# Kernel optimization log

Hardware: AMD Instinct MI355X
Metric: run time of the kernel (lower is better)

Reference implementation:

```python
import jax, jax.numpy as jnp
import numpy as np

H = 16
D_MODEL = 1024
D_K = D_MODEL // H
NWORDS = 16384


def setup_inputs() -> dict:
    key0 = jax.random.key(0)
    ks = jax.random.split(key0, 11)
    s = 0.02
    return {
        "query": jax.random.normal(ks[0], (1, D_MODEL), dtype=jnp.float32),
        "key": jax.random.normal(ks[1], (NWORDS, D_MODEL), dtype=jnp.float32),
        "value": jax.random.normal(ks[2], (NWORDS, D_MODEL), dtype=jnp.float32),
        "Wq": jax.random.normal(ks[3], (D_MODEL, D_MODEL), dtype=jnp.float32) * s,
        "bq": jax.random.normal(ks[4], (D_MODEL,), dtype=jnp.float32) * s,
        "Wk": jax.random.normal(ks[5], (D_MODEL, D_MODEL), dtype=jnp.float32) * s,
        "bk": jax.random.normal(ks[6], (D_MODEL,), dtype=jnp.float32) * s,
        "Wv": jax.random.normal(ks[7], (D_MODEL, D_MODEL), dtype=jnp.float32) * s,
        "bv": jax.random.normal(ks[8], (D_MODEL,), dtype=jnp.float32) * s,
        "Wo": jax.random.normal(ks[9], (D_MODEL, D_MODEL), dtype=jnp.float32) * s,
        "bo": jax.random.normal(ks[10], (D_MODEL,), dtype=jnp.float32) * s,
    }


def reference(query, key, value, Wq, bq, Wk, bk, Wv, bv, Wo, bo):
    # torch Linear: y = x @ W.T + b
    q = (query @ Wq.T + bq).reshape(H, D_K)          # [h, d_k]  (single query token)
    k = (key @ Wk.T + bk).reshape(-1, H, D_K)        # [n, h, d_k]
    v = (value @ Wv.T + bv).reshape(-1, H, D_K)      # [n, h, d_k]
    # NOTE: original module applies NO 1/sqrt(d_k) scaling.
    scores = jnp.einsum("hd,nhd->hn", q, k)          # [h, n]
    p_attn = jax.nn.softmax(scores, axis=-1)          # dropout p=0 -> no-op
    x = jnp.einsum("hn,nhd->hd", p_attn, v).reshape(1, H * D_K)  # [1, d_model]
    return x @ Wo.T + bo                              # [1, d_model]
```

## Files before the change

kernel.cpp:

```cpp
#include <hip/hip_runtime.h>

#define DM 1024
#define NW 16384

typedef __attribute__((ext_vector_type(8))) short short8;
typedef __attribute__((ext_vector_type(4))) float f32x4;

#define OFF_AH   1024
#define OFF_AL   9216
#define OFF_D0   17408
#define OFF_S    17424
#define OFF_X    17696
#define OFF_W    18720
#define OFF_PART 36864

__device__ __forceinline__ unsigned short f2bf(float f) {
  unsigned int u = __float_as_uint(f);
  return (unsigned short)((u + 0x7fffu + ((u >> 16) & 1u)) >> 16);
}

__global__ __launch_bounds__(256) void k_rowdot(const float* __restrict__ W,
                                                const float* __restrict__ v,
                                                const float* __restrict__ b,
                                                float* __restrict__ out) {
  const int wave = (blockIdx.x * 256 + threadIdx.x) >> 6;
  const int lane = threadIdx.x & 63;
  const float* row = W + (size_t)wave * DM + 4 * lane;
  float s = 0.f;
#pragma unroll
  for (int j = 0; j < 4; ++j) {
    float4 a = *(const float4*)(row + j * 256);
    float4 x = *(const float4*)(v + j * 256 + 4 * lane);
    s += a.x * x.x + a.y * x.y + a.z * x.z + a.w * x.w;
  }
#pragma unroll
  for (int off = 32; off; off >>= 1) s += __shfl_xor(s, off, 64);
  if (lane == 0) out[wave] = s + b[wave];
}

__global__ __launch_bounds__(256) void k_qck(const float* __restrict__ Wq,
                                             const float* __restrict__ bq,
                                             const float* __restrict__ query,
                                             const float* __restrict__ Wk,
                                             const float* __restrict__ bk,
                                             short* __restrict__ Ah,
                                             short* __restrict__ Al,
                                             float* __restrict__ d0,
                                             float* __restrict__ S,
                                             float* __restrict__ w) {
  const int h = blockIdx.x >> 2;
  const int mc = blockIdx.x & 3;
  const int t = threadIdx.x;
  const int lane = t & 63;
  const int wv = t >> 6;
  __shared__ float qh[64];
  if (blockIdx.x == 0 && t < 16) S[t] = 0.f;
  w[blockIdx.x * 256 + t] = 0.f;
  float4 qv[4];
#pragma unroll
  for (int j = 0; j < 4; ++j) qv[j] = *(const float4*)(query + j * 256 + 4 * lane);
#pragma unroll 1
  for (int ii = 0; ii < 16; ii += 4) {
    float4 a[4][4];
#pragma unroll
    for (int r = 0; r < 4; ++r) {
      const float* rp = Wq + (size_t)(h * 64 + 4 * (ii + r) + wv) * DM + 4 * lane;
#pragma unroll
      for (int j = 0; j < 4; ++j) a[r][j] = *(const float4*)(rp + j * 256);
    }
    float s[4] = {0.f, 0.f, 0.f, 0.f};
#pragma unroll
    for (int r = 0; r < 4; ++r)
#pragma unroll
      for (int j = 0; j < 4; ++j)
        s[r] += a[r][j].x * qv[j].x + a[r][j].y * qv[j].y +
                a[r][j].z * qv[j].z + a[r][j].w * qv[j].w;
#pragma unroll
    for (int off = 32; off; off >>= 1)
#pragma unroll
      for (int r = 0; r < 4; ++r) s[r] += __shfl_xor(s[r], off, 64);
    if (lane == 0)
#pragma unroll
      for (int r = 0; r < 4; ++r)
        qh[4 * (ii + r) + wv] = s[r] + bq[h * 64 + 4 * (ii + r) + wv];
  }
  __syncthreads();
  const int m = mc * 256 + t;
  const float* Wp = Wk + (size_t)(h * 64) * DM + m;
  float s = 0.f;
#pragma unroll 2
  for (int db = 0; db < 8; ++db) {
    float wv8[8];
#pragma unroll
    for (int j = 0; j < 8; ++j) wv8[j] = Wp[(size_t)(db * 8 + j) * DM];
#pragma unroll
    for (int j = 0; j < 8; ++j) s = fmaf(qh[db * 8 + j], wv8[j], s);
  }
  unsigned short hu = f2bf(s);
  float hf = __uint_as_float(((unsigned int)hu) << 16);
  unsigned short lu = f2bf(s - hf);
  const int kb = m >> 5, q = (m >> 3) & 3, j = m & 7;
  const int idx = (kb * 64 + q * 16 + h) * 8 + j;
  Ah[idx] = (short)hu;
  Al[idx] = (short)lu;
  if (mc == 0 && t == 0) {
    float tt = 0.f;
    for (int d = 0; d < 64; ++d) tt += qh[d] * bk[h * 64 + d];
    d0[h] = tt;
  }
}

__global__ __launch_bounds__(256, 1) void k_spv(const float* __restrict__ key,
                                                const float* __restrict__ value,
                                                const short* __restrict__ AhG,
                                                const short* __restrict__ AlG,
                                                const float* __restrict__ d0,
                                                float* __restrict__ part,
                                                float* __restrict__ S) {
  const int nb = blockIdx.x;
  const int t = threadIdx.x;
  const int lane = t & 63;
  const int wv = t >> 6;
  const int nl = wv * 16 + (lane & 15);
  const int n = nb * 64 + nl;
  const int quad = lane >> 4;
  const float* base = key + (size_t)n * DM + quad * 8;
  const short8* A8h = (const short8*)AhG;
  const short8* A8l = (const short8*)AlG;
  __shared__ float el[64 * 16];

  short8 ah[2][4], al[2][4];
  float4 f0[2][4], f1[2][4];
  f32x4 acc0 = {0.f, 0.f, 0.f, 0.f};
  f32x4 acc1 = {0.f, 0.f, 0.f, 0.f};

#define LOADG(buf, g) { \
  _Pragma("unroll") for (int i = 0; i < 4; ++i) { \
    const int kb = (g) * 4 + i; \
    ah[buf][i] = A8h[kb * 64 + lane]; \
    al[buf][i] = A8l[kb * 64 + lane]; \
    f0[buf][i] = *(const float4*)(base + kb * 32); \
    f1[buf][i] = *(const float4*)(base + kb * 32 + 4); \
  } }

#define PROC(buf) { \
  _Pragma("unroll") for (int i = 0; i < 4; ++i) { \
    float ff[8] = {f0[buf][i].x, f0[buf][i].y, f0[buf][i].z, f0[buf][i].w, \
                   f1[buf][i].x, f1[buf][i].y, f1[buf][i].z, f1[buf][i].w}; \
    short8 bh, bl; \
    _Pragma("unroll") for (int j = 0; j < 8; ++j) { \
      unsigned short hu = f2bf(ff[j]); \
      bh[j] = (short)hu; \
      float hf = __uint_as_float(((unsigned int)hu) << 16); \
      bl[j] = (short)f2bf(ff[j] - hf); \
    } \
    if ((i & 1) == 0) { \
      acc0 = __builtin_amdgcn_mfma_f32_16x16x32_bf16(ah[buf][i], bh, acc0, 0, 0, 0); \
      acc0 = __builtin_amdgcn_mfma_f32_16x16x32_bf16(ah[buf][i], bl, acc0, 0, 0, 0); \
      acc0 = __builtin_amdgcn_mfma_f32_16x16x32_bf16(al[buf][i], bh, acc0, 0, 0, 0); \
    } else { \
      acc1 = __builtin_amdgcn_mfma_f32_16x16x32_bf16(ah[buf][i], bh, acc1, 0, 0, 0); \
      acc1 = __builtin_amdgcn_mfma_f32_16x16x32_bf16(ah[buf][i], bl, acc1, 0, 0, 0); \
      acc1 = __builtin_amdgcn_mfma_f32_16x16x32_bf16(al[buf][i], bh, acc1, 0, 0, 0); \
    } \
  } }

  LOADG(0, 0)
  LOADG(1, 1)
  PROC(0) LOADG(0, 2)
  PROC(1) LOADG(1, 3)
  PROC(0) LOADG(0, 4)
  PROC(1) LOADG(1, 5)
  PROC(0) LOADG(0, 6)
  PROC(1) LOADG(1, 7)
  PROC(0)
  PROC(1)
#undef LOADG
#undef PROC

  {
    const float4 dv = *(const float4*)(d0 + quad * 4);
    float ex0 = __expf(acc0[0] + acc1[0] + dv.x);
    float ex1 = __expf(acc0[1] + acc1[1] + dv.y);
    float ex2 = __expf(acc0[2] + acc1[2] + dv.z);
    float ex3 = __expf(acc0[3] + acc1[3] + dv.w);
    *(float4*)&el[nl * 16 + quad * 4] = make_float4(ex0, ex1, ex2, ex3);
  }
  __syncthreads();

  float4 acc[16];
#pragma unroll
  for (int h = 0; h < 16; ++h) acc[h] = make_float4(0.f, 0.f, 0.f, 0.f);
  const float* vp = value + (size_t)(nb * 64) * DM + 4 * t;
#pragma unroll 1
  for (int rb = 0; rb < 8; ++rb) {
    float4 v[8];
#pragma unroll
    for (int i = 0; i < 8; ++i) v[i] = *(const float4*)(vp + (size_t)(rb * 8 + i) * DM);
#pragma unroll
    for (int i = 0; i < 8; ++i) {
      const float4* er4 = (const float4*)&el[(rb * 8 + i) * 16];
      float4 e0 = er4[0], e1 = er4[1], e2 = er4[2], e3 = er4[3];
      float4 vv = v[i];
#define FMA4H(H, P) { acc[H].x = fmaf(P, vv.x, acc[H].x); acc[H].y = fmaf(P, vv.y, acc[H].y); \
                      acc[H].z = fmaf(P, vv.z, acc[H].z); acc[H].w = fmaf(P, vv.w, acc[H].w); }
      FMA4H(0,  e0.x) FMA4H(1,  e0.y) FMA4H(2,  e0.z) FMA4H(3,  e0.w)
      FMA4H(4,  e1.x) FMA4H(5,  e1.y) FMA4H(6,  e1.z) FMA4H(7,  e1.w)
      FMA4H(8,  e2.x) FMA4H(9,  e2.y) FMA4H(10, e2.z) FMA4H(11, e2.w)
      FMA4H(12, e3.x) FMA4H(13, e3.y) FMA4H(14, e3.z) FMA4H(15, e3.w)
#undef FMA4H
    }
  }
  float* pp = part + (size_t)nb * (16 * DM) + 4 * t;
#pragma unroll
  for (int h = 0; h < 16; ++h) *(float4*)(pp + (size_t)h * DM) = acc[h];

  if (t < 16) {
    float s = 0.f;
#pragma unroll
    for (int r = 0; r < 64; ++r) s += el[r * 16 + t];
    atomicAdd(S + t, s);
  }
}

__global__ __launch_bounds__(256) void k_wred(const float* __restrict__ part,
                                              float* __restrict__ w) {
  const int g = blockIdx.x * 256 + threadIdx.x;
  const int o = g & 16383;
  const int q = g >> 14;
  float s = 0.f;
#pragma unroll 1
  for (int ib = 0; ib < 8; ++ib) {
    float x[8];
#pragma unroll
    for (int j = 0; j < 8; ++j)
      x[j] = part[(size_t)(q * 64 + ib * 8 + j) * 16384 + o];
#pragma unroll
    for (int j = 0; j < 8; ++j) s += x[j];
  }
  atomicAdd(w + o, s);
}

__global__ __launch_bounds__(256) void k_xproj(const float* __restrict__ Wv,
                                               const float* __restrict__ w,
                                               const float* __restrict__ bv,
                                               const float* __restrict__ S,
                                               float* __restrict__ x) {
  const int wave = (blockIdx.x * 256 + threadIdx.x) >> 6;
  const int lane = threadIdx.x & 63;
  const int h = wave >> 6;
  const float* vec = w + (size_t)h * DM;
  const float* row = Wv + (size_t)wave * DM + 4 * lane;
  float s = 0.f;
#pragma unroll
  for (int j = 0; j < 4; ++j) {
    float4 a = *(const float4*)(row + j * 256);
    float4 x4 = *(const float4*)(vec + j * 256 + 4 * lane);
    s += a.x * x4.x + a.y * x4.y + a.z * x4.z + a.w * x4.w;
  }
#pragma unroll
  for (int off = 32; off; off >>= 1) s += __shfl_xor(s, off, 64);
  if (lane == 0) x[wave] = s / S[h] + bv[wave];
}

extern "C" void kernel_launch(void* const* d_in, const int* in_sizes, int n_in,
                              void* d_out, int out_size, void* d_ws, size_t ws_size,
                              hipStream_t stream) {
  const float* query = (const float*)d_in[0];
  const float* key   = (const float*)d_in[1];
  const float* value = (const float*)d_in[2];
  const float* Wq    = (const float*)d_in[3];
  const float* bq    = (const float*)d_in[4];
  const float* Wk    = (const float*)d_in[5];
  const float* bk    = (const float*)d_in[6];
  const float* Wv    = (const float*)d_in[7];
  const float* bv    = (const float*)d_in[8];
  const float* Wo    = (const float*)d_in[9];
  const float* bo    = (const float*)d_in[10];
  float* out = (float*)d_out;
  float* ws  = (float*)d_ws;
  short* Ah  = (short*)(ws + OFF_AH);
  short* Al  = (short*)(ws + OFF_AL);

  k_qck    <<<64,  256, 0, stream>>>(Wq, bq, query, Wk, bk, Ah, Al,
                                     ws + OFF_D0, ws + OFF_S, ws + OFF_W);
  k_spv    <<<256, 256, 0, stream>>>(key, value, Ah, Al, ws + OFF_D0,
                                     ws + OFF_PART, ws + OFF_S);
  k_wred   <<<256, 256, 0, stream>>>(ws + OFF_PART, ws + OFF_W);
  k_xproj  <<<256, 256, 0, stream>>>(Wv, ws + OFF_W, bv, ws + OFF_S, ws + OFF_X);
  k_rowdot <<<256, 256, 0, stream>>>(Wo, ws + OFF_X, bo, out);
}
```

Before: 216.9 us.

## Fuse all attention stages into one cooperative kernel with grid syncs

```diff
diff --git a/kernel.cpp b/kernel.cpp
--- a/kernel.cpp
+++ b/kernel.cpp
@@ -1,4 +1,7 @@
 #include <hip/hip_runtime.h>
+#include <hip/hip_cooperative_groups.h>
+
+namespace cg = cooperative_groups;
 
 #define DM 1024
 #define NW 16384
@@ -6,139 +9,128 @@
 typedef __attribute__((ext_vector_type(8))) short short8;
 typedef __attribute__((ext_vector_type(4))) float f32x4;
 
+#define OFF_QH   0
 #define OFF_AH   1024
 #define OFF_AL   9216
 #define OFF_D0   17408
 #define OFF_S    17424
-#define OFF_X    17696
-#define OFF_W    18720
-#define OFF_PART 36864
+#define OFF_SP   17440
+#define OFF_X    21536
+#define OFF_W    22560
+#define OFF_PART 40960
 
 __device__ __forceinline__ unsigned short f2bf(float f) {
   unsigned int u = __float_as_uint(f);
   return (unsigned short)((u + 0x7fffu + ((u >> 16) & 1u)) >> 16);
 }
 
-__global__ __launch_bounds__(256) void k_rowdot(const float* __restrict__ W,
-                                                const float* __restrict__ v,
-                                                const float* __restrict__ b,
-                                                float* __restrict__ out) {
-  const int wave = (blockIdx.x * 256 + threadIdx.x) >> 6;
-  const int lane = threadIdx.x & 63;
-  const float* row = W + (size_t)wave * DM + 4 * lane;
-  float s = 0.f;
-#pragma unroll
-  for (int j = 0; j < 4; ++j) {
-    float4 a = *(const float4*)(row + j * 256);
-    float4 x = *(const float4*)(v + j * 256 + 4 * lane);
-    s += a.x * x.x + a.y * x.y + a.z * x.z + a.w * x.w;
-  }
-#pragma unroll
-  for (int off = 32; off; off >>= 1) s += __shfl_xor(s, off, 64);
-  if (lane == 0) out[wave] = s + b[wave];
-}
-
-__global__ __launch_bounds__(256) void k_qck(const float* __restrict__ Wq,
-                                             const float* __restrict__ bq,
-                                             const float* __restrict__ query,
-                                             const float* __restrict__ Wk,
-                                             const float* __restrict__ bk,
-                                             short* __restrict__ Ah,
-                                             short* __restrict__ Al,
-                                             float* __restrict__ d0,
-                                             float* __restrict__ S,
-                                             float* __restrict__ w) {
-  const int h = blockIdx.x >> 2;
-  const int mc = blockIdx.x & 3;
+__global__ __launch_bounds__(512, 2) void k_fused(
+    const float* __restrict__ query, const float* __restrict__ key,
+    const float* __restrict__ value, const float* __restrict__ Wq,
+    const float* __restrict__ bq, const float* __restrict__ Wk,
+    const float* __restrict__ bk, const float* __restrict__ Wv,
+    const float* __restrict__ bv, const float* __restrict__ Wo,
+    const float* __restrict__ bo, float* __restrict__ out,
+    float* __restrict__ ws) {
+  cg::grid_group grid = cg::this_grid();
+  const int b = blockIdx.x;
   const int t = threadIdx.x;
   const int lane = t & 63;
   const int wv = t >> 6;
-  __shared__ float qh[64];
-  if (blockIdx.x == 0 && t < 16) S[t] = 0.f;
-  w[blockIdx.x * 256 + t] = 0.f;
-  float4 qv[4];
-#pragma unroll
-  for (int j = 0; j < 4; ++j) qv[j] = *(const float4*)(query + j * 256 + 4 * lane);
-#pragma unroll 1
-  for (int ii = 0; ii < 16; ii += 4) {
-    float4 a[4][4];
-#pragma unroll
-    for (int r = 0; r < 4; ++r) {
-      const float* rp = Wq + (size_t)(h * 64 + 4 * (ii + r) + wv) * DM + 4 * lane;
-#pragma unroll
-      for (int j = 0; j < 4; ++j) a[r][j] = *(const float4*)(rp + j * 256);
-    }
-    float s[4] = {0.f, 0.f, 0.f, 0.f};
-#pragma unroll
-    for (int r = 0; r < 4; ++r)
-#pragma unroll
-      for (int j = 0; j < 4; ++j)
-        s[r] += a[r][j].x * qv[j].x + a[r][j].y * qv[j].y +
-                a[r][j].z * qv[j].z + a[r][j].w * qv[j].w;
-#pragma unroll
-    for (int off = 32; off; off >>= 1)
-#pragma unroll
-      for (int r = 0; r < 4; ++r) s[r] += __shfl_xor(s[r], off, 64);
-    if (lane == 0)
-#pragma unroll
-      for (int r = 0; r < 4; ++r)
-        qh[4 * (ii + r) + wv] = s[r] + bq[h * 64 + 4 * (ii + r) + wv];
-  }
-  __syncthreads();
-  const int m = mc * 256 + t;
-  const float* Wp = Wk + (size_t)(h * 64) * DM + m;
-  float s = 0.f;
-#pragma unroll 2
-  for (int db = 0; db < 8; ++db) {
-    float wv8[8];
-#pragma unroll
-    for (int j = 0; j < 8; ++j) wv8[j] = Wp[(size_t)(db * 8 + j) * DM];
-#pragma unroll
-    for (int j = 0; j < 8; ++j) s = fmaf(qh[db * 8 + j], wv8[j], s);
-  }
-  unsigned short hu = f2bf(s);
-  float hf = __uint_as_float(((unsigned int)hu) << 16);
-  unsigned short lu = f2bf(s - hf);
-  const int kb = m >> 5, q = (m >> 3) & 3, j = m & 7;
-  const int idx = (kb * 64 + q * 16 + h) * 8 + j;
-  Ah[idx] = (short)hu;
-  Al[idx] = (short)lu;
-  if (mc == 0 && t == 0) {
-    float tt = 0.f;
-    for (int d = 0; d < 64; ++d) tt += qh[d] * bk[h * 64 + d];
-    d0[h] = tt;
-  }
-}
-
-__global__ __launch_bounds__(256, 1) void k_spv(const float* __restrict__ key,
-                                                const float* __restrict__ value,
-                                                const short* __restrict__ AhG,
-                                                const short* __restrict__ AlG,
-                                                const float* __restrict__ d0,
-                                                float* __restrict__ part,
-                                                float* __restrict__ S) {
-  const int nb = blockIdx.x;
-  const int t = threadIdx.x;
-  const int lane = t & 63;
-  const int wv = t >> 6;
-  const int nl = wv * 16 + (lane & 15);
-  const int n = nb * 64 + nl;
-  const int quad = lane >> 4;
-  const float* base = key + (size_t)n * DM + quad * 8;
-  const short8* A8h = (const short8*)AhG;
-  const short8* A8l = (const short8*)AlG;
+
+  float* qh_g  = ws + OFF_QH;
+  short* Ah    = (short*)(ws + OFF_AH);
+  short* Al    = (short*)(ws + OFF_AL);
+  float* d0    = ws + OFF_D0;
+  float* Sg    = ws + OFF_S;
+  float* Spart = ws + OFF_SP;
+  float* xg    = ws + OFF_X;
+  float* wg    = ws + OFF_W;
+  float* part  = ws + OFF_PART;
+
+  __shared__ float pr[8];
+  __shared__ float qsh[64];
+  __shared__ float cred[8][64];
   __shared__ float el[64 * 16];
-
-  short8 ah[2][4], al[2][4];
-  float4 f0[2][4], f1[2][4];
-  f32x4 acc0 = {0.f, 0.f, 0.f, 0.f};
-  f32x4 acc1 = {0.f, 0.f, 0.f, 0.f};
+  __shared__ f32x4 sred[8][64];
+  __shared__ float wr[8][64];
+
+  {
+    const int row = b * 4 + (wv >> 1);
+    const int half = wv & 1;
+    const float* rp = Wq + (size_t)row * DM + 4 * lane;
+    float s = 0.f;
+#pragma unroll
+    for (int j = 0; j < 2; ++j) {
+      const int off = (half * 2 + j) * 256;
+      float4 a = *(const float4*)(rp + off);
+      float4 x = *(const float4*)(query + off + 4 * lane);
+      s += a.x * x.x + a.y * x.y + a.z * x.z + a.w * x.w;
+    }
+#pragma unroll
+    for (int off = 32; off; off >>= 1) s += __shfl_xor(s, off, 64);
+    if (lane == 0) pr[wv] = s;
+    __syncthreads();
+    if (t < 4) qh_g[b * 4 + t] = pr[2 * t] + pr[2 * t + 1] + bq[b * 4 + t];
+  }
+  grid.sync();
+
+  {
+    const int h = b >> 4;
+    const int seg = b & 15;
+    if (t < 64) qsh[t] = qh_g[h * 64 + t];
+    __syncthreads();
+    const int col = seg * 64 + lane;
+    const float* wp = Wk + (size_t)(h * 64 + wv * 8) * DM + col;
+    float s = 0.f;
+#pragma unroll
+    for (int jj = 0; jj < 8; ++jj)
+      s = fmaf(qsh[wv * 8 + jj], wp[(size_t)jj * DM], s);
+    cred[wv][lane] = s;
+    if (seg == 0 && wv == 1) {
+      float p = qsh[lane] * bk[h * 64 + lane];
+#pragma unroll
+      for (int off = 32; off; off >>= 1) p += __shfl_xor(p, off, 64);
+      if (lane == 0) d0[h] = p;
+    }
+    __syncthreads();
+    if (wv == 0) {
+      float c = 0.f;
+#pragma unroll
+      for (int g = 0; g < 8; ++g) c += cred[g][lane];
+      unsigned short hu = f2bf(c);
+      float hf = __uint_as_float(((unsigned int)hu) << 16);
+      unsigned short lu = f2bf(c - hf);
+      const int m = col;
+      const int kb = m >> 5, q = (m >> 3) & 3, j = m & 7;
+      const int idx = (kb * 64 + q * 16 + h) * 8 + j;
+      Ah[idx] = (short)hu;
+      Al[idx] = (short)lu;
+    }
+  }
+  grid.sync();
+
+  {
+    const int nb = b;
+    const int tile = wv >> 1;
+    const int khalf = wv & 1;
+    const int nl = tile * 16 + (lane & 15);
+    const int n = nb * 64 + nl;
+    const int quad = lane >> 4;
+    const float* base = key + (size_t)n * DM + quad * 8;
+    const short8* A8h = (const short8*)Ah;
+    const short8* A8l = (const short8*)Al;
+
+    short8 ahf[2][4], alf[2][4];
+    float4 f0[2][4], f1[2][4];
+    f32x4 acc0 = {0.f, 0.f, 0.f, 0.f};
+    f32x4 acc1 = {0.f, 0.f, 0.f, 0.f};
 
 #define LOADG(buf, g) { \
   _Pragma("unroll") for (int i = 0; i < 4; ++i) { \
-    const int kb = (g) * 4 + i; \
-    ah[buf][i] = A8h[kb * 64 + lane]; \
-    al[buf][i] = A8l[kb * 64 + lane]; \
+    const int kb = khalf * 16 + (g) * 4 + i; \
+    ahf[buf][i] = A8h[kb * 64 + lane]; \
+    alf[buf][i] = A8l[kb * 64 + lane]; \
     f0[buf][i] = *(const float4*)(base + kb * 32); \
     f1[buf][i] = *(const float4*)(base + kb * 32 + 4); \
   } }
@@ -155,112 +147,147 @@
       bl[j] = (short)f2bf(ff[j] - hf); \
     } \
     if ((i & 1) == 0) { \
-      acc0 = __builtin_amdgcn_mfma_f32_16x16x32_bf16(ah[buf][i], bh, acc0, 0, 0, 0); \
-      acc0 = __builtin_amdgcn_mfma_f32_16x16x32_bf16(ah[buf][i], bl, acc0, 0, 0, 0); \
-      acc0 = __builtin_amdgcn_mfma_f32_16x16x32_bf16(al[buf][i], bh, acc0, 0, 0, 0); \
+      acc0 = __builtin_amdgcn_mfma_f32_16x16x32_bf16(ahf[buf][i], bh, acc0, 0, 0, 0); \
+      acc0 = __builtin_amdgcn_mfma_f32_16x16x32_bf16(ahf[buf][i], bl, acc0, 0, 0, 0); \
+      acc0 = __builtin_amdgcn_mfma_f32_16x16x32_bf16(alf[buf][i], bh, acc0, 0, 0, 0); \
     } else { \
-      acc1 = __builtin_amdgcn_mfma_f32_16x16x32_bf16(ah[buf][i], bh, acc1, 0, 0, 0); \
-      acc1 = __builtin_amdgcn_mfma_f32_16x16x32_bf16(ah[buf][i], bl, acc1, 0, 0, 0); \
-      acc1 = __builtin_amdgcn_mfma_f32_16x16x32_bf16(al[buf][i], bh, acc1, 0, 0, 0); \
+      acc1 = __builtin_amdgcn_mfma_f32_16x16x32_bf16(ahf[buf][i], bh, acc1, 0, 0, 0); \
+      acc1 = __builtin_amdgcn_mfma_f32_16x16x32_bf16(ahf[buf][i], bl, acc1, 0, 0, 0); \
+      acc1 = __builtin_amdgcn_mfma_f32_16x16x32_bf16(alf[buf][i], bh, acc1, 0, 0, 0); \
     } \
   } }
 
-  LOADG(0, 0)
-  LOADG(1, 1)
-  PROC(0) LOADG(0, 2)
-  PROC(1) LOADG(1, 3)
-  PROC(0) LOADG(0, 4)
-  PROC(1) LOADG(1, 5)
-  PROC(0) LOADG(0, 6)
-  PROC(1) LOADG(1, 7)
-  PROC(0)
-  PROC(1)
+    LOADG(0, 0)
+    LOADG(1, 1)
+    PROC(0) LOADG(0, 2)
+    PROC(1) LOADG(1, 3)
+    PROC(0)
+    PROC(1)
 #undef LOADG
 #undef PROC
 
-  {
-    const float4 dv = *(const float4*)(d0 + quad * 4);
-    float ex0 = __expf(acc0[0] + acc1[0] + dv.x);
-    float ex1 = __expf(acc0[1] + acc1[1] + dv.y);
-    float ex2 = __expf(acc0[2] + acc1[2] + dv.z);
-    float ex3 = __expf(acc0[3] + acc1[3] + dv.w);
-    *(float4*)&el[nl * 16 + quad * 4] = make_float4(ex0, ex1, ex2, ex3);
-  }
-  __syncthreads();
-
-  float4 acc[16];
-#pragma unroll
-  for (int h = 0; h < 16; ++h) acc[h] = make_float4(0.f, 0.f, 0.f, 0.f);
-  const float* vp = value + (size_t)(nb * 64) * DM + 4 * t;
+    f32x4 at = acc0 + acc1;
+    sred[wv][lane] = at;
+    __syncthreads();
+    if (khalf == 0) {
+      f32x4 o = sred[wv + 1][lane];
+      const float4 dv = *(const float4*)(d0 + quad * 4);
+      float ex0 = __expf(at[0] + o[0] + dv.x);
+      float ex1 = __expf(at[1] + o[1] + dv.y);
+      float ex2 = __expf(at[2] + o[2] + dv.z);
+      float ex3 = __expf(at[3] + o[3] + dv.w);
+      *(float4*)&el[nl * 16 + quad * 4] = make_float4(ex0, ex1, ex2, ex3);
+    }
+    __syncthreads();
+    if (t < 16) {
+      float s = 0.f;
+#pragma unroll
+      for (int r = 0; r < 64; ++r) s += el[r * 16 + t];
+      Spart[nb * 16 + t] = s;
+    }
+    float2 acc[16];
+#pragma unroll
+    for (int h = 0; h < 16; ++h) acc[h] = make_float2(0.f, 0.f);
+    const float* vp = value + (size_t)(nb * 64) * DM + 2 * t;
 #pragma unroll 1
-  for (int rb = 0; rb < 8; ++rb) {
-    float4 v[8];
-#pragma unroll
-    for (int i = 0; i < 8; ++i) v[i] = *(const float4*)(vp + (size_t)(rb * 8 + i) * DM);
-#pragma unroll
-    for (int i = 0; i < 8; ++i) {
-      const float4* er4 = (const float4*)&el[(rb * 8 + i) * 16];
-      float4 e0 = er4[0], e1 = er4[1], e2 = er4[2], e3 = er4[3];
-      float4 vv = v[i];
-#define FMA4H(H, P) { acc[H].x = fmaf(P, vv.x, acc[H].x); acc[H].y = fmaf(P, vv.y, acc[H].y); \
-                      acc[H].z = fmaf(P, vv.z, acc[H].z); acc[H].w = fmaf(P, vv.w, acc[H].w); }
-      FMA4H(0,  e0.x) FMA4H(1,  e0.y) FMA4H(2,  e0.z) FMA4H(3,  e0.w)
-      FMA4H(4,  e1.x) FMA4H(5,  e1.y) FMA4H(6,  e1.z) FMA4H(7,  e1.w)
-      FMA4H(8,  e2.x) FMA4H(9,  e2.y) FMA4H(10, e2.z) FMA4H(11, e2.w)
-      FMA4H(12, e3.x) FMA4H(13, e3.y) FMA4H(14, e3.z) FMA4H(15, e3.w)
-#undef FMA4H
-    }
-  }
-  float* pp = part + (size_t)nb * (16 * DM) + 4 * t;
-#pragma unroll
-  for (int h = 0; h < 16; ++h) *(float4*)(pp + (size_t)h * DM) = acc[h];
-
-  if (t < 16) {
-    float s = 0.f;
-#pragma unroll
-    for (int r = 0; r < 64; ++r) s += el[r * 16 + t];
-    atomicAdd(S + t, s);
-  }
-}
-
-__global__ __launch_bounds__(256) void k_wred(const float* __restrict__ part,
-                                              float* __restrict__ w) {
-  const int g = blockIdx.x * 256 + threadIdx.x;
-  const int o = g & 16383;
-  const int q = g >> 14;
-  float s = 0.f;
+    for (int rb = 0; rb < 8; ++rb) {
+      float2 v[8];
+#pragma unroll
+      for (int i = 0; i < 8; ++i) v[i] = *(const float2*)(vp + (size_t)(rb * 8 + i) * DM);
+#pragma unroll
+      for (int i = 0; i < 8; ++i) {
+        const float4* er4 = (const float4*)&el[(rb * 8 + i) * 16];
+        float4 e0 = er4[0], e1 = er4[1], e2 = er4[2], e3 = er4[3];
+        float2 vvv = v[i];
+#define F2H(H, P) { acc[H].x = fmaf(P, vvv.x, acc[H].x); acc[H].y = fmaf(P, vvv.y, acc[H].y); }
+        F2H(0,  e0.x) F2H(1,  e0.y) F2H(2,  e0.z) F2H(3,  e0.w)
+        F2H(4,  e1.x) F2H(5,  e1.y) F2H(6,  e1.z) F2H(7,  e1.w)
+        F2H(8,  e2.x) F2H(9,  e2.y) F2H(10, e2.z) F2H(11, e2.w)
+        F2H(12, e3.x) F2H(13, e3.y) F2H(14, e3.z) F2H(15, e3.w)
+#undef F2H
+      }
+    }
+    float* pp = part + (size_t)nb * (16 * DM) + 2 * t;
+#pragma unroll
+    for (int h = 0; h < 16; ++h) *(float2*)(pp + (size_t)h * DM) = acc[h];
+  }
+  grid.sync();
+
+  {
+    const int col = b * 64 + lane;
+    float s = 0.f;
 #pragma unroll 1
-  for (int ib = 0; ib < 8; ++ib) {
-    float x[8];
-#pragma unroll
-    for (int j = 0; j < 8; ++j)
-      x[j] = part[(size_t)(q * 64 + ib * 8 + j) * 16384 + o];
-#pragma unroll
-    for (int j = 0; j < 8; ++j) s += x[j];
-  }
-  atomicAdd(w + o, s);
-}
-
-__global__ __launch_bounds__(256) void k_xproj(const float* __restrict__ Wv,
-                                               const float* __restrict__ w,
-                                               const float* __restrict__ bv,
-                                               const float* __restrict__ S,
-                                               float* __restrict__ x) {
-  const int wave = (blockIdx.x * 256 + threadIdx.x) >> 6;
-  const int lane = threadIdx.x & 63;
-  const int h = wave >> 6;
-  const float* vec = w + (size_t)h * DM;
-  const float* row = Wv + (size_t)wave * DM + 4 * lane;
-  float s = 0.f;
-#pragma unroll
-  for (int j = 0; j < 4; ++j) {
-    float4 a = *(const float4*)(row + j * 256);
-    float4 x4 = *(const float4*)(vec + j * 256 + 4 * lane);
-    s += a.x * x4.x + a.y * x4.y + a.z * x4.z + a.w * x4.w;
-  }
-#pragma unroll
-  for (int off = 32; off; off >>= 1) s += __shfl_xor(s, off, 64);
-  if (lane == 0) x[wave] = s / S[h] + bv[wave];
+    for (int ib = 0; ib < 4; ++ib) {
+      float x[8];
+#pragma unroll
+      for (int j = 0; j < 8; ++j)
+        x[j] = part[(size_t)(wv * 32 + ib * 8 + j) * 16384 + col];
+#pragma unroll
+      for (int j = 0; j < 8; ++j) s += x[j];
+    }
+    wr[wv][lane] = s;
+    if (b < 16 && t < 256) {
+      float p = Spart[t * 16 + b];
+#pragma unroll
+      for (int off = 32; off; off >>= 1) p += __shfl_xor(p, off, 64);
+      if (lane == 0) pr[wv] = p;
+    }
+    __syncthreads();
+    if (wv == 0) {
+      float c = 0.f;
+#pragma unroll
+      for (int g = 0; g < 8; ++g) c += wr[g][lane];
+      wg[col] = c;
+    }
+    if (b < 16 && t == 0) Sg[b] = pr[0] + pr[1] + pr[2] + pr[3];
+  }
+  grid.sync();
+
+  {
+    const int row = b * 4 + (wv >> 1);
+    const int half = wv & 1;
+    const float* rp = Wv + (size_t)row * DM + 4 * lane;
+    const float* vec = wg + (size_t)(row >> 6) * DM;
+    float s = 0.f;
+#pragma unroll
+    for (int j = 0; j < 2; ++j) {
+      const int off = (half * 2 + j) * 256;
+      float4 a = *(const float4*)(rp + off);
+      float4 x = *(const float4*)(vec + off + 4 * lane);
+      s += a.x * x.x + a.y * x.y + a.z * x.z + a.w * x.w;
+    }
+#pragma unroll
+    for (int off = 32; off; off >>= 1) s += __shfl_xor(s, off, 64);
+    if (lane == 0) pr[wv] = s;
+    __syncthreads();
+    if (t < 4) {
+      const int r = b * 4 + t;
+      xg[r] = (pr[2 * t] + pr[2 * t + 1]) / Sg[r >> 6] + bv[r];
+    }
+  }
+  grid.sync();
+
+  {
+    const int row = b * 4 + (wv >> 1);
+    const int half = wv & 1;
+    const float* rp = Wo + (size_t)row * DM + 4 * lane;
+    float s = 0.f;
+#pragma unroll
+    for (int j = 0; j < 2; ++j) {
+      const int off = (half * 2 + j) * 256;
+      float4 a = *(const float4*)(rp + off);
+      float4 x = *(const float4*)(xg + off + 4 * lane);
+      s += a.x * x.x + a.y * x.y + a.z * x.z + a.w * x.w;
+    }
+#pragma unroll
+    for (int off = 32; off; off >>= 1) s += __shfl_xor(s, off, 64);
+    if (lane == 0) pr[wv] = s;
+    __syncthreads();
+    if (t < 4) {
+      const int r = b * 4 + t;
+      out[r] = pr[2 * t] + pr[2 * t + 1] + bo[r];
+    }
+  }
 }
 
 extern "C" void kernel_launch(void* const* d_in, const int* in_sizes, int n_in,
@@ -279,14 +306,10 @@
   const float* bo    = (const float*)d_in[10];
   float* out = (float*)d_out;
   float* ws  = (float*)d_ws;
-  short* Ah  = (short*)(ws + OFF_AH);
-  short* Al  = (short*)(ws + OFF_AL);
-
-  k_qck    <<<64,  256, 0, stream>>>(Wq, bq, query, Wk, bk, Ah, Al,
-                                     ws + OFF_D0, ws + OFF_S, ws + OFF_W);
-  k_spv    <<<256, 256, 0, stream>>>(key, value, Ah, Al, ws + OFF_D0,
-                                     ws + OFF_PART, ws + OFF_S);
-  k_wred   <<<256, 256, 0, stream>>>(ws + OFF_PART, ws + OFF_W);
-  k_xproj  <<<256, 256, 0, stream>>>(Wv, ws + OFF_W, bv, ws + OFF_S, ws + OFF_X);
-  k_rowdot <<<256, 256, 0, stream>>>(Wo, ws + OFF_X, bo, out);
+
+  void* args[] = {(void*)&query, (void*)&key, (void*)&value, (void*)&Wq,
+                  (void*)&bq,    (void*)&Wk,  (void*)&bk,    (void*)&Wv,
+                  (void*)&bv,    (void*)&Wo,  (void*)&bo,    (void*)&out,
+                  (void*)&ws};
+  hipLaunchCooperativeKernel((void*)k_fused, dim3(256), dim3(512), args, 0, stream);
 }
```

Measured after the change: 350.8 us. +61.7%, slower.

## Halve rows per score block, split K across wave pairs, double-buffer value loads

Applied to the files above, without the earlier changes.

```diff
diff --git a/kernel.cpp b/kernel.cpp
--- a/kernel.cpp
+++ b/kernel.cpp
@@ -9,10 +9,10 @@
 #define OFF_AH   1024
 #define OFF_AL   9216
 #define OFF_D0   17408
-#define OFF_S    17424
-#define OFF_X    17696
-#define OFF_W    18720
-#define OFF_PART 36864
+#define OFF_SP   17440
+#define OFF_X    25632
+#define OFF_W    26656
+#define OFF_PART 49152
 
 __device__ __forceinline__ unsigned short f2bf(float f) {
   unsigned int u = __float_as_uint(f);
@@ -46,7 +46,6 @@
                                              short* __restrict__ Ah,
                                              short* __restrict__ Al,
                                              float* __restrict__ d0,
-                                             float* __restrict__ S,
                                              float* __restrict__ w) {
   const int h = blockIdx.x >> 2;
   const int mc = blockIdx.x & 3;
@@ -54,7 +53,6 @@
   const int lane = t & 63;
   const int wv = t >> 6;
   __shared__ float qh[64];
-  if (blockIdx.x == 0 && t < 16) S[t] = 0.f;
   w[blockIdx.x * 256 + t] = 0.f;
   float4 qv[4];
 #pragma unroll
@@ -110,24 +108,27 @@
   }
 }
 
-__global__ __launch_bounds__(256, 1) void k_spv(const float* __restrict__ key,
+__global__ __launch_bounds__(256, 2) void k_spv(const float* __restrict__ key,
                                                 const float* __restrict__ value,
                                                 const short* __restrict__ AhG,
                                                 const short* __restrict__ AlG,
                                                 const float* __restrict__ d0,
                                                 float* __restrict__ part,
-                                                float* __restrict__ S) {
+                                                float* __restrict__ Spart) {
   const int nb = blockIdx.x;
   const int t = threadIdx.x;
   const int lane = t & 63;
   const int wv = t >> 6;
-  const int nl = wv * 16 + (lane & 15);
-  const int n = nb * 64 + nl;
+  const int tile = wv >> 1;
+  const int khalf = wv & 1;
+  const int nl = tile * 16 + (lane & 15);
+  const int n = nb * 32 + nl;
   const int quad = lane >> 4;
   const float* base = key + (size_t)n * DM + quad * 8;
   const short8* A8h = (const short8*)AhG;
   const short8* A8l = (const short8*)AlG;
-  __shared__ float el[64 * 16];
+  __shared__ float el[32 * 16];
+  __shared__ f32x4 sred[4][64];
 
   short8 ah[2][4], al[2][4];
   float4 f0[2][4], f1[2][4];
@@ -136,7 +137,7 @@
 
 #define LOADG(buf, g) { \
   _Pragma("unroll") for (int i = 0; i < 4; ++i) { \
-    const int kb = (g) * 4 + i; \
+    const int kb = khalf * 16 + (g) * 4 + i; \
     ah[buf][i] = A8h[kb * 64 + lane]; \
     al[buf][i] = A8l[kb * 64 + lane]; \
     f0[buf][i] = *(const float4*)(base + kb * 32); \
@@ -169,58 +170,92 @@
   LOADG(1, 1)
   PROC(0) LOADG(0, 2)
   PROC(1) LOADG(1, 3)
-  PROC(0) LOADG(0, 4)
-  PROC(1) LOADG(1, 5)
-  PROC(0) LOADG(0, 6)
-  PROC(1) LOADG(1, 7)
   PROC(0)
   PROC(1)
 #undef LOADG
 #undef PROC
 
-  {
+  f32x4 at = acc0 + acc1;
+  sred[wv][lane] = at;
+  __syncthreads();
+  if (khalf == 0) {
+    f32x4 o = sred[wv + 1][lane];
     const float4 dv = *(const float4*)(d0 + quad * 4);
-    float ex0 = __expf(acc0[0] + acc1[0] + dv.x);
-    float ex1 = __expf(acc0[1] + acc1[1] + dv.y);
-    float ex2 = __expf(acc0[2] + acc1[2] + dv.z);
-    float ex3 = __expf(acc0[3] + acc1[3] + dv.w);
+    float ex0 = __expf(at[0] + o[0] + dv.x);
+    float ex1 = __expf(at[1] + o[1] + dv.y);
+    float ex2 = __expf(at[2] + o[2] + dv.z);
+    float ex3 = __expf(at[3] + o[3] + dv.w);
     *(float4*)&el[nl * 16 + quad * 4] = make_float4(ex0, ex1, ex2, ex3);
   }
   __syncthreads();
-
-  float4 acc[16];
-#pragma unroll
-  for (int h = 0; h < 16; ++h) acc[h] = make_float4(0.f, 0.f, 0.f, 0.f);
-  const float* vp = value + (size_t)(nb * 64) * DM + 4 * t;
-#pragma unroll 1
-  for (int rb = 0; rb < 8; ++rb) {
-    float4 v[8];
-#pragma unroll
-    for (int i = 0; i < 8; ++i) v[i] = *(const float4*)(vp + (size_t)(rb * 8 + i) * DM);
-#pragma unroll
-    for (int i = 0; i < 8; ++i) {
-      const float4* er4 = (const float4*)&el[(rb * 8 + i) * 16];
-      float4 e0 = er4[0], e1 = er4[1], e2 = er4[2], e3 = er4[3];
-      float4 vv = v[i];
-#define FMA4H(H, P) { acc[H].x = fmaf(P, vv.x, acc[H].x); acc[H].y = fmaf(P, vv.y, acc[H].y); \
-                      acc[H].z = fmaf(P, vv.z, acc[H].z); acc[H].w = fmaf(P, vv.w, acc[H].w); }
-      FMA4H(0,  e0.x) FMA4H(1,  e0.y) FMA4H(2,  e0.z) FMA4H(3,  e0.w)
-      FMA4H(4,  e1.x) FMA4H(5,  e1.y) FMA4H(6,  e1.z) FMA4H(7,  e1.w)
-      FMA4H(8,  e2.x) FMA4H(9,  e2.y) FMA4H(10, e2.z) FMA4H(11, e2.w)
-      FMA4H(12, e3.x) FMA4H(13, e3.y) FMA4H(14, e3.z) FMA4H(15, e3.w)
-#undef FMA4H
-    }
-  }
-  float* pp = part + (size_t)nb * (16 * DM) + 4 * t;
-#pragma unroll
-  for (int h = 0; h < 16; ++h) *(float4*)(pp + (size_t)h * DM) = acc[h];
-
   if (t < 16) {
     float s = 0.f;
 #pragma unroll
-    for (int r = 0; r < 64; ++r) s += el[r * 16 + t];
-    atomicAdd(S + t, s);
-  }
+    for (int r = 0; r < 32; ++r) s += el[r * 16 + t];
+    Spart[t * 512 + nb] = s;
+  }
+
+  float4 acc[16];
+#pragma unroll
+  for (int h = 0; h < 16; ++h) acc[h] = make_float4(0.f, 0.f, 0.f, 0.f);
+  const float* vp = value + (size_t)(nb * 32) * DM + 4 * t;
+  float4 vbuf[2][8];
+
+#define LOADV(buf, g) { \
+  _Pragma("unroll") for (int i = 0; i < 8; ++i) \
+    vbuf[buf][i] = *(const float4*)(vp + (size_t)((g) * 8 + i) * DM); }
+
+#define COMPV(buf, g) { \
+  _Pragma("unroll") for (int i = 0; i < 8; ++i) { \
+    const float4* er4 = (const float4*)&el[((g) * 8 + i) * 16]; \
+    float4 e0 = er4[0], e1 = er4[1], e2 = er4[2], e3 = er4[3]; \
+    float4 vvv = vbuf[buf][i]; \
+    acc[0].x  = fmaf(e0.x, vvv.x, acc[0].x);  acc[0].y  = fmaf(e0.x, vvv.y, acc[0].y); \
+    acc[0].z  = fmaf(e0.x, vvv.z, acc[0].z);  acc[0].w  = fmaf(e0.x, vvv.w, acc[0].w); \
+    acc[1].x  = fmaf(e0.y, vvv.x, acc[1].x);  acc[1].y  = fmaf(e0.y, vvv.y, acc[1].y); \
+    acc[1].z  = fmaf(e0.y, vvv.z, acc[1].z);  acc[1].w  = fmaf(e0.y, vvv.w, acc[1].w); \
+    acc[2].x  = fmaf(e0.z, vvv.x, acc[2].x);  acc[2].y  = fmaf(e0.z, vvv.y, acc[2].y); \
+    acc[2].z  = fmaf(e0.z, vvv.z, acc[2].z);  acc[2].w  = fmaf(e0.z, vvv.w, acc[2].w); \
+    acc[3].x  = fmaf(e0.w, vvv.x, acc[3].x);  acc[3].y  = fmaf(e0.w, vvv.y, acc[3].y); \
+    acc[3].z  = fmaf(e0.w, vvv.z, acc[3].z);  acc[3].w  = fmaf(e0.w, vvv.w, acc[3].w); \
+    acc[4].x  = fmaf(e1.x, vvv.x, acc[4].x);  acc[4].y  = fmaf(e1.x, vvv.y, acc[4].y); \
+    acc[4].z  = fmaf(e1.x, vvv.z, acc[4].z);  acc[4].w  = fmaf(e1.x, vvv.w, acc[4].w); \
+    acc[5].x  = fmaf(e1.y, vvv.x, acc[5].x);  acc[5].y  = fmaf(e1.y, vvv.y, acc[5].y); \
+    acc[5].z  = fmaf(e1.y, vvv.z, acc[5].z);  acc[5].w  = fmaf(e1.y, vvv.w, acc[5].w); \
+    acc[6].x  = fmaf(e1.z, vvv.x, acc[6].x);  acc[6].y  = fmaf(e1.z, vvv.y, acc[6].y); \
+    acc[6].z  = fmaf(e1.z, vvv.z, acc[6].z);  acc[6].w  = fmaf(e1.z, vvv.w, acc[6].w); \
+    acc[7].x  = fmaf(e1.w, vvv.x, acc[7].x);  acc[7].y  = fmaf(e1.w, vvv.y, acc[7].y); \
+    acc[7].z  = fmaf(e1.w, vvv.z, acc[7].z);  acc[7].w  = fmaf(e1.w, vvv.w, acc[7].w); \
+    acc[8].x  = fmaf(e2.x, vvv.x, acc[8].x);  acc[8].y  = fmaf(e2.x, vvv.y, acc[8].y); \
+    acc[8].z  = fmaf(e2.x, vvv.z, acc[8].z);  acc[8].w  = fmaf(e2.x, vvv.w, acc[8].w); \
+    acc[9].x  = fmaf(e2.y, vvv.x, acc[9].x);  acc[9].y  = fmaf(e2.y, vvv.y, acc[9].y); \
+    acc[9].z  = fmaf(e2.y, vvv.z, acc[9].z);  acc[9].w  = fmaf(e2.y, vvv.w, acc[9].w); \
+    acc[10].x = fmaf(e2.z, vvv.x, acc[10].x); acc[10].y = fmaf(e2.z, vvv.y, acc[10].y); \
+    acc[10].z = fmaf(e2.z, vvv.z, acc[10].z); acc[10].w = fmaf(e2.z, vvv.w, acc[10].w); \
+    acc[11].x = fmaf(e2.w, vvv.x, acc[11].x); acc[11].y = fmaf(e2.w, vvv.y, acc[11].y); \
+    acc[11].z = fmaf(e2.w, vvv.z, acc[11].z); acc[11].w = fmaf(e2.w, vvv.w, acc[11].w); \
+    acc[12].x = fmaf(e3.x, vvv.x, acc[12].x); acc[12].y = fmaf(e3.x, vvv.y, acc[12].y); \
+    acc[12].z = fmaf(e3.x, vvv.z, acc[12].z); acc[12].w = fmaf(e3.x, vvv.w, acc[12].w); \
+    acc[13].x = fmaf(e3.y, vvv.x, acc[13].x); acc[13].y = fmaf(e3.y, vvv.y, acc[13].y); \
+    acc[13].z = fmaf(e3.y, vvv.z, acc[13].z); acc[13].w = fmaf(e3.y, vvv.w, acc[13].w); \
+    acc[14].x = fmaf(e3.z, vvv.x, acc[14].x); acc[14].y = fmaf(e3.z, vvv.y, acc[14].y); \
+    acc[14].z = fmaf(e3.z, vvv.z, acc[14].z); acc[14].w = fmaf(e3.z, vvv.w, acc[14].w); \
+    acc[15].x = fmaf(e3.w, vvv.x, acc[15].x); acc[15].y = fmaf(e3.w, vvv.y, acc[15].y); \
+    acc[15].z = fmaf(e3.w, vvv.z, acc[15].z); acc[15].w = fmaf(e3.w, vvv.w, acc[15].w); \
+  } }
+
+  LOADV(0, 0)
+  LOADV(1, 1)
+  COMPV(0, 0) LOADV(0, 2)
+  COMPV(1, 1) LOADV(1, 3)
+  COMPV(0, 2)
+  COMPV(1, 3)
+#undef LOADV
+#undef COMPV
+
+  float* pp = part + (size_t)nb * (16 * DM) + 4 * t;
+#pragma unroll
+  for (int h = 0; h < 16; ++h) *(float4*)(pp + (size_t)h * DM) = acc[h];
 }
 
 __global__ __launch_bounds__(256) void k_wred(const float* __restrict__ part,
@@ -230,11 +265,11 @@
   const int q = g >> 14;
   float s = 0.f;
 #pragma unroll 1
-  for (int ib = 0; ib < 8; ++ib) {
+  for (int ib = 0; ib < 16; ++ib) {
     float x[8];
 #pragma unroll
     for (int j = 0; j < 8; ++j)
-      x[j] = part[(size_t)(q * 64 + ib * 8 + j) * 16384 + o];
+      x[j] = part[(size_t)(q * 128 + ib * 8 + j) * 16384 + o];
 #pragma unroll
     for (int j = 0; j < 8; ++j) s += x[j];
   }
@@ -244,14 +279,17 @@
 __global__ __launch_bounds__(256) void k_xproj(const float* __restrict__ Wv,
                                                const float* __restrict__ w,
                                                const float* __restrict__ bv,
-                                               const float* __restrict__ S,
+                                               const float* __restrict__ Spart,
                                                float* __restrict__ x) {
   const int wave = (blockIdx.x * 256 + threadIdx.x) >> 6;
   const int lane = threadIdx.x & 63;
   const int h = wave >> 6;
   const float* vec = w + (size_t)h * DM;
   const float* row = Wv + (size_t)wave * DM + 4 * lane;
-  float s = 0.f;
+  const float* sp = Spart + (size_t)h * 512;
+  float s = 0.f, ss = 0.f;
+#pragma unroll
+  for (int i = 0; i < 8; ++i) ss += sp[i * 64 + lane];
 #pragma unroll
   for (int j = 0; j < 4; ++j) {
     float4 a = *(const float4*)(row + j * 256);
@@ -259,8 +297,11 @@
     s += a.x * x4.x + a.y * x4.y + a.z * x4.z + a.w * x4.w;
   }
 #pragma unroll
-  for (int off = 32; off; off >>= 1) s += __shfl_xor(s, off, 64);
-  if (lane == 0) x[wave] = s / S[h] + bv[wave];
+  for (int off = 32; off; off >>= 1) {
+    s += __shfl_xor(s, off, 64);
+    ss += __shfl_xor(ss, off, 64);
+  }
+  if (lane == 0) x[wave] = s / ss + bv[wave];
 }
 
 extern "C" void kernel_launch(void* const* d_in, const int* in_sizes, int n_in,
@@ -283,10 +324,10 @@
   short* Al  = (short*)(ws + OFF_AL);
 
   k_qck    <<<64,  256, 0, stream>>>(Wq, bq, query, Wk, bk, Ah, Al,
-                                     ws + OFF_D0, ws + OFF_S, ws + OFF_W);
-  k_spv    <<<256, 256, 0, stream>>>(key, value, Ah, Al, ws + OFF_D0,
-                                     ws + OFF_PART, ws + OFF_S);
+                                     ws + OFF_D0, ws + OFF_W);
+  k_spv    <<<512, 256, 0, stream>>>(key, value, Ah, Al, ws + OFF_D0,
+                                     ws + OFF_PART, ws + OFF_SP);
   k_wred   <<<256, 256, 0, stream>>>(ws + OFF_PART, ws + OFF_W);
-  k_xproj  <<<256, 256, 0, stream>>>(Wv, ws + OFF_W, bv, ws + OFF_S, ws + OFF_X);
+  k_xproj  <<<256, 256, 0, stream>>>(Wv, ws + OFF_W, bv, ws + OFF_SP, ws + OFF_X);
   k_rowdot <<<256, 256, 0, stream>>>(Wo, ws + OFF_X, bo, out);
 }
```

Result: faster. 208.8 us (-3.7%).
